# Optimization experiments

Measured on AMD Instinct MI355X. Metric: run time of the kernel, lower is better.

## Reference

```python
import jax, jax.numpy as jnp
import numpy as np

B, N, C, K = 2, 4096, 128, 16
EPS = 1e-5


def _conv(w, b, x):
    # 1x1 Conv2d == per-point channel mix: w [O,I], x [B,I,N,K]
    return jnp.einsum('oi,bink->bonk', w, x) + b[None, :, None, None]


def _bn(x, g, be):
    # training-mode BatchNorm2d: biased stats over (B, N, K) per channel
    m = jnp.mean(x, axis=(0, 2, 3), keepdims=True)
    v = jnp.var(x, axis=(0, 2, 3), keepdims=True)
    return g[None, :, None, None] * (x - m) * jax.lax.rsqrt(v + EPS) + be[None, :, None, None]


def setup_inputs() -> dict:
    key = jax.random.key(0)
    ks = jax.random.split(key, 24)

    def w(k_, o, i):
        return jax.random.normal(k_, (o, i), jnp.float32) * (1.0 / np.sqrt(i))

    def b(k_, o):
        return jax.random.normal(k_, (o,), jnp.float32) * 0.01

    return {
        'xyz': jax.random.normal(ks[0], (B, 3, N), jnp.float32),
        'features': jax.random.normal(ks[1], (B, C, N), jnp.float32),
        'w_theta1': w(ks[2], C, 3), 'b_theta1': b(ks[3], C),
        'w_theta2': w(ks[4], C, C), 'b_theta2': b(ks[5], C),
        'g_theta': jnp.ones((C,), jnp.float32), 'beta_theta': jnp.zeros((C,), jnp.float32),
        'w_phi': w(ks[6], C, C), 'b_phi': b(ks[7], C),
        'w_psi': w(ks[8], C, C), 'b_psi': b(ks[9], C),
        'w_alpha': w(ks[10], C, C), 'b_alpha': b(ks[11], C),
        'w_gamma1': w(ks[12], C, C), 'b_gamma1': b(ks[13], C),
        'w_gamma2': w(ks[14], C, C), 'b_gamma2': b(ks[15], C),
        'g_gamma': jnp.ones((C,), jnp.float32), 'beta_gamma': jnp.zeros((C,), jnp.float32),
        'k': K,
    }


def reference(xyz, features, w_theta1, b_theta1, w_theta2, b_theta2, g_theta, beta_theta,
              w_phi, b_phi, w_psi, b_psi, w_alpha, b_alpha,
              w_gamma1, b_gamma1, w_gamma2, b_gamma2, g_gamma, beta_gamma, k):
    Bv, _, Nv = xyz.shape
    # --- knn on coordinates: negative squared distances, top-k neighbors ---
    xx = jnp.sum(xyz * xyz, axis=1, keepdims=True)                 # [B,1,N]
    inner = -2.0 * jnp.einsum('bcn,bcm->bnm', xyz, xyz)            # [B,N,N]
    dist = -xx - inner - jnp.swapaxes(xx, 1, 2)                    # -||xi-xj||^2
    idx = jax.lax.top_k(dist, k)[1]                                # [B,N,K]

    bidx = jnp.arange(Bv)[:, None, None]
    xt = jnp.swapaxes(xyz, 1, 2)                                   # [B,N,3]
    nbr_x = xt[bidx, idx]                                          # [B,N,K,3]
    pos = jnp.transpose(xt[:, :, None, :] - nbr_x, (0, 3, 1, 2))   # [B,3,N,K]
    ft = jnp.swapaxes(features, 1, 2)                              # [B,N,C]
    x_j = jnp.transpose(ft[bidx, idx], (0, 3, 1, 2))               # [B,C,N,K]

    # delta = relu(BN(theta2(theta1(pos))))
    delta = jax.nn.relu(_bn(_conv(w_theta2, b_theta2, _conv(w_theta1, b_theta1, pos)), g_theta, beta_theta))
    # phi(x_i): conv is per-point, so compute on [B,C,N] and broadcast over K
    lin_xi = (jnp.einsum('oi,bin->bon', w_phi, features) + b_phi[None, :, None])[..., None]
    lin_xj = _conv(w_psi, b_psi, x_j)
    rel = lin_xi - lin_xj + delta
    rel = jax.nn.relu(_bn(_conv(w_gamma2, b_gamma2, _conv(w_gamma1, b_gamma1, rel)), g_gamma, beta_gamma))
    weights = jax.nn.softmax(rel, axis=-1)                         # softmax over K
    feats = _conv(w_alpha, b_alpha, x_j) + delta
    return jnp.sum(weights * feats, axis=-1)                       # [B,C,N]
```

## Files before the change

kernel.cpp:

```cpp
#include <hip/hip_runtime.h>
#include <math.h>

typedef __attribute__((ext_vector_type(8))) short short8;
typedef __attribute__((ext_vector_type(4))) float f32x4;
typedef unsigned short u16;
typedef unsigned long long u64;

#define NNPTS 131072
#define NQ    8192

__device__ __forceinline__ u16 f2bf(float f) {
  unsigned u = __float_as_uint(f);
  u = u + 0x7fffu + ((u >> 16) & 1u);
  return (u16)(u >> 16);
}
__device__ __forceinline__ float bf2f(u16 h) {
  return __uint_as_float(((unsigned)h) << 16);
}
__device__ __forceinline__ unsigned fkey(float f) {
  unsigned u = __float_as_uint(f);
  return u ^ (((unsigned)((int)u >> 31)) | 0x80000000u);
}

__device__ __forceinline__ unsigned wave_max_u32(unsigned v) {
  unsigned t;
  t = (unsigned)__builtin_amdgcn_update_dpp(0, (int)v, 0x111, 0xf, 0xf, true); v = v > t ? v : t;
  t = (unsigned)__builtin_amdgcn_update_dpp(0, (int)v, 0x112, 0xf, 0xf, true); v = v > t ? v : t;
  t = (unsigned)__builtin_amdgcn_update_dpp(0, (int)v, 0x114, 0xf, 0xf, true); v = v > t ? v : t;
  t = (unsigned)__builtin_amdgcn_update_dpp(0, (int)v, 0x118, 0xf, 0xf, true); v = v > t ? v : t;
  t = (unsigned)__builtin_amdgcn_update_dpp(0, (int)v, 0x142, 0xf, 0xf, true); v = v > t ? v : t;
  t = (unsigned)__builtin_amdgcn_update_dpp(0, (int)v, 0x143, 0xf, 0xf, true); v = v > t ? v : t;
  return (unsigned)__builtin_amdgcn_readlane((int)v, 63);
}

__global__ __launch_bounds__(256) void front_kernel(
    const float* __restrict__ xyz, const float* __restrict__ f,
    const float* __restrict__ wphi, const float* __restrict__ wpsi,
    const float* __restrict__ walpha,
    const float* __restrict__ wg1, const float* __restrict__ wg2,
    const float* __restrict__ bg1, const float* __restrict__ bg2,
    const float* __restrict__ wt1, const float* __restrict__ bt1,
    const float* __restrict__ wt2, const float* __restrict__ bt2,
    u16* __restrict__ featB,
    u16* __restrict__ WphiB, u16* __restrict__ WpsiB, u16* __restrict__ WalphaB,
    u16* __restrict__ WfusB, float* __restrict__ c0v,
    float* __restrict__ Wc, float* __restrict__ bc,
    int* __restrict__ idxOut)
{
  __shared__ float sh[4160];
  int bid = blockIdx.x, tid = threadIdx.x;

  if (bid < 2048) {
    float* xxS = sh;
    int lane = tid & 63, wid = tid >> 6;
    int q = bid*4 + wid;
    int b = q >> 12, n = q & 4095;
    const float* X = xyz + (size_t)b * 12288;
    for (int t = tid; t < 4096; t += 256) {
      float mx = X[t], my = X[4096+t], mz = X[8192+t];
      xxS[t] = __fadd_rn(__fadd_rn(__fmul_rn(mx,mx), __fmul_rn(my,my)), __fmul_rn(mz,mz));
    }
    __syncthreads();
    float qx = X[n], qy = X[4096+n], qz = X[8192+n];
    float xxq = xxS[n];

    float v0=-INFINITY, v1=-INFINITY, v2=-INFINITY, v3=-INFINITY;
    int   i0=0x7fffffff, i1=0x7fffffff, i2=0x7fffffff, i3=0x7fffffff;
    u64 alive = ~0ull;

    #pragma unroll 8
    for (int j = 0; j < 64; ++j) {
      int m = j*64 + lane;
      float mx = X[m], my = X[4096+m], mz = X[8192+m];
      float xxm = xxS[m];
      float dot = __fadd_rn(__fadd_rn(__fmul_rn(qx,mx), __fmul_rn(qy,my)), __fmul_rn(qz,mz));
      float inner = __fmul_rn(-2.0f, dot);
      float dv = __fsub_rn(__fsub_rn(-xxm, inner), xxq);
      bool c0_=dv>v0, c1_=dv>v1, c2_=dv>v2, c3_=dv>v3;
      int ni1 = c0_ ? i0 : (c1_ ? m : i1);
      int ni2 = c1_ ? i1 : (c2_ ? m : i2);
      int ni3 = c2_ ? i2 : (c3_ ? m : i3);
      i0 = c0_ ? m : i0;
      i1 = ni1; i2 = ni2; i3 = ni3;
      float nv1 = __builtin_amdgcn_fmed3f(dv, v0, v1);
      float nv2 = __builtin_amdgcn_fmed3f(dv, v1, v2);
      float nv3 = __builtin_amdgcn_fmed3f(dv, v2, v3);
      v0 = fmaxf(v0, dv);
      v1 = nv1; v2 = nv2; v3 = nv3;
    }

    int cnt = 4;
    for (int r = 0; r < 16; ++r) {
      unsigned hi = fkey(v0);
      unsigned ghi = wave_max_u32(hi);
      u64 bal = __ballot(hi == ghi);
      unsigned gi;
      if (__builtin_popcountll(bal) == 1) {
        int ln = (int)__builtin_ctzll(bal);
        gi = (unsigned)__builtin_amdgcn_readlane(i0, ln);
      } else {
        unsigned lo = (hi == ghi) ? (0xFFFFFFFFu - (unsigned)i0) : 0u;
        gi = 0xFFFFFFFFu - wave_max_u32(lo);
      }
      if (lane == 0) idxOut[(size_t)q*16 + r] = (int)gi;
      if ((int)(gi & 63) == lane) {
        alive &= ~(1ull << (gi >> 6));
        v0=v1; i0=i1; v1=v2; i1=i2; v2=v3; i2=i3; v3=-INFINITY; i3=0x7fffffff;
        if (--cnt == 0 && r < 15) {
          v0=v1=v2=v3=-INFINITY; i0=i1=i2=i3=0x7fffffff;
          for (int j2 = 0; j2 < 64; ++j2) {
            if (!((alive >> j2) & 1ull)) continue;
            int m = j2*64 + lane;
            float mx = X[m], my = X[4096+m], mz = X[8192+m];
            float xxm = xxS[m];
            float dot = __fadd_rn(__fadd_rn(__fmul_rn(qx,mx), __fmul_rn(qy,my)), __fmul_rn(qz,mz));
            float inner = __fmul_rn(-2.0f, dot);
            float dv = __fsub_rn(__fsub_rn(-xxm, inner), xxq);
            bool c0_=dv>v0, c1_=dv>v1, c2_=dv>v2, c3_=dv>v3;
            int ni1 = c0_ ? i0 : (c1_ ? m : i1);
            int ni2 = c1_ ? i1 : (c2_ ? m : i2);
            int ni3 = c2_ ? i2 : (c3_ ? m : i3);
            i0 = c0_ ? m : i0;
            i1 = ni1; i2 = ni2; i3 = ni3;
            float nv1 = __builtin_amdgcn_fmed3f(dv, v0, v1);
            float nv2 = __builtin_amdgcn_fmed3f(dv, v1, v2);
            float nv3 = __builtin_amdgcn_fmed3f(dv, v2, v3);
            v0 = fmaxf(v0, dv);
            v1 = nv1; v2 = nv2; v3 = nv3;
          }
          cnt = 4;
        }
      }
    }
  } else if (bid < 2304) {
    float (*T)[65] = (float(*)[65])sh;
    int t = bid - 2048;
    int tx = tid & 63, tg = tid >> 6;
    int n0 = (t & 63) * 64, c0_ = ((t >> 6) & 1) * 64, b = t >> 7;
    const float* src = f + ((size_t)b * 128 + c0_) * 4096 + n0;
    #pragma unroll
    for (int it = 0; it < 16; ++it) {
      int cl = tg + it * 4;
      T[cl][tx] = src[(size_t)cl * 4096 + tx];
    }
    __syncthreads();
    u16* dst = featB + ((size_t)b * 4096 + n0) * 128 + c0_;
    #pragma unroll
    for (int it = 0; it < 16; ++it) {
      int nl = tg + it * 4;
      dst[(size_t)nl * 128 + tx] = f2bf(T[tx][nl]);
    }
  } else {
    int cc = bid - 2304;
    if (tid < 128) {
      int i = tid;
      WphiB[cc*128+i]   = f2bf(wphi[cc*128+i]);
      WpsiB[cc*128+i]   = f2bf(wpsi[cc*128+i]);
      WalphaB[cc*128+i] = f2bf(walpha[cc*128+i]);
      float s = 0.f;
      for (int t = 0; t < 128; ++t) s = fmaf(wg2[cc*128+t], wg1[t*128+i], s);
      WfusB[cc*128+i] = f2bf(s);
      if (i == 0) {
        float s0 = bg2[cc];
        for (int t = 0; t < 128; ++t) s0 = fmaf(wg2[cc*128+t], bg1[t], s0);
        c0v[cc] = s0;
        for (int j = 0; j < 3; ++j) {
          float a = 0.f;
          for (int t = 0; t < 128; ++t) a = fmaf(wt2[cc*128+t], wt1[t*3+j], a);
          Wc[cc*3+j] = a;
        }
        float bb = bt2[cc];
        for (int t = 0; t < 128; ++t) bb = fmaf(wt2[cc*128+t], bt1[t], bb);
        bc[cc] = bb;
      }
    }
  }
}

__device__ __forceinline__ void theta_fold_c(const double* __restrict__ stS,
                                             const float* __restrict__ Wc,
                                             const float* __restrict__ bc,
                                             const float* __restrict__ gth,
                                             const float* __restrict__ bth,
                                             int c, float* w0o, float* w1o,
                                             float* w2o, float* bdo)
{
  const double cnt = (double)NNPTS;
  double m0 = stS[0]/cnt, m1 = stS[1]/cnt, m2 = stS[2]/cnt;
  double Pxx = stS[3]/cnt, Pxy = stS[4]/cnt, Pxz = stS[5]/cnt;
  double Pyy = stS[6]/cnt, Pyz = stS[7]/cnt, Pzz = stS[8]/cnt;
  double w0 = Wc[c*3], w1 = Wc[c*3+1], w2 = Wc[c*3+2], bb = bc[c];
  double wm = w0*m0 + w1*m1 + w2*m2;
  double mu = wm + bb;
  double quad = w0*(Pxx*w0 + Pxy*w1 + Pxz*w2)
              + w1*(Pxy*w0 + Pyy*w1 + Pyz*w2)
              + w2*(Pxz*w0 + Pyz*w1 + Pzz*w2);
  double Ex2 = quad + 2.0*bb*wm + bb*bb;
  double var = Ex2 - mu*mu;
  double s = (double)gth[c] / sqrt(var + 1e-5);
  double t = (double)bth[c] - s*mu;
  *w0o = (float)(s*w0);
  *w1o = (float)(s*w1);
  *w2o = (float)(s*w2);
  *bdo = (float)(s*bb + t);
}

__device__ __forceinline__ void zero_acc(f32x4 a[2][4]) {
  #pragma unroll
  for (int mt = 0; mt < 2; ++mt)
    #pragma unroll
    for (int nt = 0; nt < 4; ++nt)
      a[mt][nt] = (f32x4){0.f, 0.f, 0.f, 0.f};
}

__device__ __forceinline__ void load_af(const u16* __restrict__ WB, int m0, int row, int g,
                                        short8 a[2][4]) {
  #pragma unroll
  for (int mt = 0; mt < 2; ++mt)
    #pragma unroll
    for (int kc = 0; kc < 4; ++kc)
      a[mt][kc] = *(const short8*)&WB[(size_t)(m0 + mt*16 + row)*128 + kc*32 + g*8];
}

__device__ __forceinline__ void gemm64(const short8 a[2][4], const uint4* __restrict__ Xs4,
                                       int row, int g, f32x4 acc[2][4]) {
  #pragma unroll
  for (int kc = 0; kc < 4; ++kc) {
    #pragma unroll
    for (int nt = 0; nt < 4; ++nt) {
      int p = nt*16 + row;
      short8 bfr = *(const short8*)&Xs4[p*16 + ((kc*4 + g) ^ (p & 7))];
      acc[0][nt] = __builtin_amdgcn_mfma_f32_16x16x32_bf16(a[0][kc], bfr, acc[0][nt], 0, 0, 0);
      acc[1][nt] = __builtin_amdgcn_mfma_f32_16x16x32_bf16(a[1][kc], bfr, acc[1][nt], 0, 0, 0);
    }
  }
}

__global__ __launch_bounds__(256) void mid_kernel(
    const u16* __restrict__ featB,
    const u16* __restrict__ WphiB, const u16* __restrict__ WpsiB,
    const u16* __restrict__ WalphaB,
    const float* __restrict__ bphi, const float* __restrict__ bpsi,
    const float* __restrict__ balpha,
    float* __restrict__ linxi, float* __restrict__ psiP, float* __restrict__ alphaP,
    const float* __restrict__ xyz, const int* __restrict__ idx,
    double* __restrict__ part)
{
  __shared__ uint4 Xs4[64*16];
  __shared__ double rd[256];
  int bid = blockIdx.x, tid = threadIdx.x;

  if (bid < 128) {
    int lane = tid & 63, wid = tid >> 6;
    int row = lane & 15, g = lane >> 4, m0 = wid * 32;
    size_t g0 = (size_t)bid * 64;
    for (int u = tid; u < 1024; u += 256) {
      int p = u >> 4, seg = u & 15;
      Xs4[p*16 + (seg ^ (p & 7))] = *(const uint4*)&featB[(g0 + p)*128 + seg*8];
    }
    __syncthreads();
    const u16* Ws[3]    = {WphiB, WpsiB, WalphaB};
    const float* bs[3]  = {bphi, bpsi, balpha};
    float* outs[3]      = {linxi, psiP, alphaP};
    #pragma unroll
    for (int w = 0; w < 3; ++w) {
      short8 afr[2][4];
      load_af(Ws[w], m0, row, g, afr);
      f32x4 acc[2][4];
      zero_acc(acc);
      gemm64(afr, Xs4, row, g, acc);
      #pragma unroll
      for (int mt = 0; mt < 2; ++mt) {
        int c = m0 + mt*16 + g*4;
        float4 bp = *(const float4*)&bs[w][c];
        const float* bpp = (const float*)&bp;
        #pragma unroll
        for (int nt = 0; nt < 4; ++nt) {
          int p = nt*16 + row;
          float4 v = make_float4(acc[mt][nt][0]+bpp[0], acc[mt][nt][1]+bpp[1],
                                 acc[mt][nt][2]+bpp[2], acc[mt][nt][3]+bpp[3]);
          *(float4*)&outs[w][(g0 + p)*128 + c] = v;
        }
      }
    }
  } else {
    int bid2 = bid - 128;
    int qg = bid2*256 + tid;
    int b = qg >> 12, n = qg & 4095;
    const float* X = xyz + (size_t)b * 12288;
    float qx = X[n], qy = X[4096+n], qz = X[8192+n];
    double l[9] = {0,0,0,0,0,0,0,0,0};
    for (int kk = 0; kk < 16; ++kk) {
      int nb = idx[(size_t)qg*16 + kk];
      float px = qx - X[nb], py = qy - X[4096+nb], pz = qz - X[8192+nb];
      l[0] += px; l[1] += py; l[2] += pz;
      l[3] += (double)px*px; l[4] += (double)px*py; l[5] += (double)px*pz;
      l[6] += (double)py*py; l[7] += (double)py*pz; l[8] += (double)pz*pz;
    }
    for (int j = 0; j < 9; ++j) {
      __syncthreads();
      rd[tid] = l[j];
      __syncthreads();
      for (int s = 128; s > 0; s >>= 1) {
        if (tid < s) rd[tid] += rd[tid + s];
        __syncthreads();
      }
      if (tid == 0) part[(size_t)bid2*9 + j] = rd[0];
    }
  }
}

__global__ __launch_bounds__(256) void gamma_part(const float* __restrict__ gs,
                                                  const float* __restrict__ gq,
                                                  double* __restrict__ partS,
                                                  double* __restrict__ partQ)
{
  int c = threadIdx.x & 127;
  int arr = threadIdx.x >> 7;
  int j = blockIdx.x;
  const float* src = arr ? gq : gs;
  double s = 0.0;
  #pragma unroll 8
  for (int bk = j*32; bk < j*32 + 32; ++bk)
    s += src[(size_t)bk*128 + c];
  (arr ? partQ : partS)[(size_t)j*128 + c] = s;
}

__global__ __launch_bounds__(256) void fused_pass(
    const float* __restrict__ psiP, const float* __restrict__ linxi,
    const int* __restrict__ idx, const float* __restrict__ xyz,
    const u16* __restrict__ WfusB, const float* __restrict__ c0,
    const double* __restrict__ part, const float* __restrict__ Wc,
    const float* __restrict__ bc, const float* __restrict__ gth,
    const float* __restrict__ bth,
    u16* __restrict__ g2W,
    float* __restrict__ gs, float* __restrict__ gq)
{
  __shared__ uint4 XsR[64*16];
  __shared__ float LxS[4][128];
  __shared__ float WdS[4][128];
  __shared__ float posS[3][64];
  __shared__ int   pidx[64];
  __shared__ float redS[128], redQ[128];
  __shared__ double stS[9];

  int tid = threadIdx.x, lane = tid & 63, wid = tid >> 6;
  int row = lane & 15, g = lane >> 4;
  int m0 = wid * 32;
  int q0 = blockIdx.x * 4, b = q0 >> 12;
  int n0 = q0 & 4095;
  const float* X = xyz + (size_t)b * 12288;
  size_t b12 = (size_t)b << 12;

  if (tid < 64) {
    int q = tid >> 4;
    int nb = idx[(size_t)(q0 + q)*16 + (tid & 15)];
    pidx[tid] = nb;
    int nq = n0 + q;
    posS[0][tid] = X[nq]      - X[nb];
    posS[1][tid] = X[4096+nq] - X[4096+nb];
    posS[2][tid] = X[8192+nq] - X[8192+nb];
  } else if (tid < 73) {
    int j = tid - 64;
    double s = 0.0;
    for (int bk = 0; bk < 32; ++bk) s += part[(size_t)bk*9 + j];
    stS[j] = s;
  }
  for (int u = tid; u < 512; u += 256)
    LxS[u >> 7][u & 127] = linxi[(size_t)q0*128 + u];
  __syncthreads();
  if (tid < 128) {
    float a0, a1, a2, a3;
    theta_fold_c(stS, Wc, bc, gth, bth, tid, &a0, &a1, &a2, &a3);
    WdS[0][tid] = a0; WdS[1][tid] = a1; WdS[2][tid] = a2; WdS[3][tid] = a3;
  }
  __syncthreads();

  #pragma unroll
  for (int it = 0; it < 4; ++it) {
    int u = tid + it*256;
    int p = u >> 4, seg = u & 15;
    int q = p >> 4, cc = seg * 8;
    float p0 = posS[0][p], p1 = posS[1][p], p2 = posS[2][p];
    const float* psir = &psiP[(b12 + (size_t)pidx[p])*128 + cc];
    float ps[8];
    *(float4*)&ps[0] = *(const float4*)&psir[0];
    *(float4*)&ps[4] = *(const float4*)&psir[4];
    ushort4 lohi[2];
    u16* wv = (u16*)lohi;
    #pragma unroll
    for (int r = 0; r < 8; ++r) {
      int c = cc + r;
      float d = fmaf(WdS[2][c], p2, fmaf(WdS[1][c], p1, fmaf(WdS[0][c], p0, WdS[3][c])));
      d = fmaxf(d, 0.f);
      wv[r] = f2bf(LxS[q][c] - ps[r] + d);
    }
    XsR[p*16 + (seg ^ (p & 7))] = *(uint4*)lohi;
  }
  __syncthreads();

  short8 afr[2][4];
  f32x4 acc[2][4];
  load_af(WfusB, m0, row, g, afr);
  zero_acc(acc);
  gemm64(afr, XsR, row, g, acc);

  #pragma unroll
  for (int mt = 0; mt < 2; ++mt) {
    int c = m0 + mt*16 + g*4;
    float4 c0v = *(const float4*)&c0[c];
    const float* c0p = (const float*)&c0v;
    float sv[4], qv[4];
    #pragma unroll
    for (int r = 0; r < 4; ++r) { sv[r] = 0.f; qv[r] = 0.f; }
    #pragma unroll
    for (int nt = 0; nt < 4; ++nt) {
      size_t gbase = ((size_t)(q0 + nt)*128 + c)*16 + row;
      #pragma unroll
      for (int r = 0; r < 4; ++r) {
        float gg = acc[mt][nt][r] + c0p[r];
        g2W[gbase + (size_t)r*16] = f2bf(gg);
        sv[r] += gg; qv[r] = fmaf(gg, gg, qv[r]);
      }
    }
    #pragma unroll
    for (int r = 0; r < 4; ++r) {
      #pragma unroll
      for (int d = 1; d < 16; d <<= 1) {
        sv[r] += __shfl_xor(sv[r], d);
        qv[r] += __shfl_xor(qv[r], d);
      }
    }
    if (row == 0) {
      *(float4*)&redS[c] = make_float4(sv[0], sv[1], sv[2], sv[3]);
      *(float4*)&redQ[c] = make_float4(qv[0], qv[1], qv[2], qv[3]);
    }
  }
  __syncthreads();
  if (tid < 128) {
    gs[(size_t)blockIdx.x*128 + tid] = redS[tid];
    gq[(size_t)blockIdx.x*128 + tid] = redQ[tid];
  }
}

__global__ __launch_bounds__(256) void out_kernel(const u16* __restrict__ g2W,
                                                  const float* __restrict__ alphaP,
                                                  const int* __restrict__ idx,
                                                  const float* __restrict__ xyz,
                                                  const double* __restrict__ part,
                                                  const float* __restrict__ Wc,
                                                  const float* __restrict__ bc,
                                                  const float* __restrict__ gth,
                                                  const float* __restrict__ bth,
                                                  const double* __restrict__ partS,
                                                  const double* __restrict__ partQ,
                                                  const float* __restrict__ gga,
                                                  const float* __restrict__ bga,
                                                  float* __restrict__ out)
{
  __shared__ int   pidxO[16][16];
  __shared__ float posO[3][16][16];
  __shared__ float prmS[6][64];
  __shared__ float resS[64][18];
  __shared__ double stS[9];
  int tid = threadIdx.x;
  int cblk = blockIdx.x & 1;
  int qblk = blockIdx.x >> 1;
  int c0 = cblk * 64;
  int lc = tid & 63;
  int c = c0 + lc;
  int qg = tid >> 6;
  int q0 = qblk * 16;
  int bb = q0 >> 12;
  int n0 = q0 & 4095;
  size_t bOff = (size_t)bb << 12;
  const float* X = xyz + (size_t)bb * 12288;
  {
    int q = tid >> 4, k = tid & 15;
    int gq = q0 + q;
    int nq = gq & 4095;
    int nb = idx[(size_t)gq*16 + k];
    pidxO[q][k] = nb;
    posO[0][q][k] = X[nq]      - X[nb];
    posO[1][q][k] = X[4096+nq] - X[4096+nb];
    posO[2][q][k] = X[8192+nq] - X[8192+nb];
  }
  if (tid < 9) {
    int j = tid;
    double s = 0.0;
    for (int bk = 0; bk < 32; ++bk) s += part[(size_t)bk*9 + j];
    stS[j] = s;
  }
  __syncthreads();
  if (tid < 64) {
    int cc = c0 + tid;
    double S = 0.0, Q = 0.0;
    #pragma unroll 8
    for (int j = 0; j < 64; ++j) {
      S += partS[(size_t)j*128 + cc];
      Q += partQ[(size_t)j*128 + cc];
    }
    const double cntd = (double)NNPTS;
    double md = S/cntd, vd = Q/cntd - md*md;
    double sd = (double)gga[cc] / sqrt(vd + 1e-5);
    prmS[0][tid] = (float)sd;
    prmS[1][tid] = (float)((double)bga[cc] - sd*md);
    float a0, a1, a2, a3;
    theta_fold_c(stS, Wc, bc, gth, bth, cc, &a0, &a1, &a2, &a3);
    prmS[2][tid] = a0; prmS[3][tid] = a1; prmS[4][tid] = a2; prmS[5][tid] = a3;
  }
  __syncthreads();
  float s  = prmS[0][lc], t   = prmS[1][lc];
  float w0 = prmS[2][lc], w1  = prmS[3][lc];
  float w2 = prmS[4][lc], bdv = prmS[5][lc];
  #pragma unroll
  for (int qi = 0; qi < 4; ++qi) {
    int ql = qi*4 + qg;
    int gq = q0 + ql;
    size_t base2 = ((size_t)gq*128 + c)*16;
    uint4 ga = *(const uint4*)&g2W[base2];
    uint4 gb = *(const uint4*)&g2W[base2 + 8];
    unsigned gw[8] = {ga.x, ga.y, ga.z, ga.w, gb.x, gb.y, gb.z, gb.w};
    float se = 0.f, so = 0.f;
    #pragma unroll
    for (int k = 0; k < 16; ++k) {
      u16 hv = (u16)((gw[k >> 1] >> ((k & 1) * 16)) & 0xFFFFu);
      float rel = fmaxf(fmaf(s, bf2f(hv), t), 0.f);
      float e = expf(rel);
      float d = fmaf(w2, posO[2][ql][k], fmaf(w1, posO[1][ql][k], fmaf(w0, posO[0][ql][k], bdv)));
      d = fmaxf(d, 0.f);
      float F = alphaP[(bOff + (size_t)pidxO[ql][k])*128 + c] + d;
      se += e; so = fmaf(e, F, so);
    }
    resS[lc][ql] = so / se;
  }
  __syncthreads();
  if (tid < 128) {
    int lc2 = tid >> 1, half = tid & 1;
    int c2 = c0 + lc2;
    float* dst = &out[(((size_t)bb*128 + c2) << 12) + n0 + half*8];
    float4 v0 = make_float4(resS[lc2][half*8+0], resS[lc2][half*8+1],
                            resS[lc2][half*8+2], resS[lc2][half*8+3]);
    float4 v1 = make_float4(resS[lc2][half*8+4], resS[lc2][half*8+5],
                            resS[lc2][half*8+6], resS[lc2][half*8+7]);
    *(float4*)&dst[0] = v0;
    *(float4*)&dst[4] = v1;
  }
}

extern "C" void kernel_launch(void* const* d_in, const int* in_sizes, int n_in,
                              void* d_out, int out_size, void* d_ws, size_t ws_size,
                              hipStream_t stream)
{
  const float* xyz      = (const float*)d_in[0];
  const float* features = (const float*)d_in[1];
  const float* wt1      = (const float*)d_in[2];
  const float* bt1      = (const float*)d_in[3];
  const float* wt2      = (const float*)d_in[4];
  const float* bt2      = (const float*)d_in[5];
  const float* gth      = (const float*)d_in[6];
  const float* bth      = (const float*)d_in[7];
  const float* wphi     = (const float*)d_in[8];
  const float* bphi     = (const float*)d_in[9];
  const float* wpsi     = (const float*)d_in[10];
  const float* bpsi     = (const float*)d_in[11];
  const float* walpha   = (const float*)d_in[12];
  const float* balpha   = (const float*)d_in[13];
  const float* wg1      = (const float*)d_in[14];
  const float* bg1      = (const float*)d_in[15];
  const float* wg2      = (const float*)d_in[16];
  const float* bg2      = (const float*)d_in[17];
  const float* gga      = (const float*)d_in[18];
  const float* bga      = (const float*)d_in[19];

  char* w = (char*)d_ws;
  size_t off = 0;
  auto take = [&](size_t bytes) -> void* {
    void* p = w + off;
    off = (off + bytes + 255) & ~(size_t)255;
    return p;
  };
  int*    idxW    = (int*)   take((size_t)NQ*16*4);
  u16*    featB   = (u16*)   take((size_t)NQ*128*2);
  float*  linxi   = (float*) take((size_t)NQ*128*4);
  float*  psiP    = (float*) take((size_t)NQ*128*4);
  float*  alphaP  = (float*) take((size_t)NQ*128*4);
  u16*    WphiB   = (u16*)   take(32768);
  u16*    WpsiB   = (u16*)   take(32768);
  u16*    WalphaB = (u16*)   take(32768);
  u16*    WfusB   = (u16*)   take(32768);
  float*  c0      = (float*) take(512);
  float*  Wc      = (float*) take(1536);
  float*  bc      = (float*) take(512);
  double* part    = (double*)take(32*9*8);
  float*  gs      = (float*) take((size_t)2048*128*4);
  float*  gq      = (float*) take((size_t)2048*128*4);
  double* partS   = (double*)take((size_t)64*128*8);
  double* partQ   = (double*)take((size_t)64*128*8);
  u16*    g2W     = (u16*)   take((size_t)NNPTS*128*2);
  float*  out     = (float*)d_out;

  front_kernel<<<2432, 256, 0, stream>>>(xyz, features,
      wphi, wpsi, walpha, wg1, wg2, bg1, bg2, wt1, bt1, wt2, bt2,
      featB, WphiB, WpsiB, WalphaB, WfusB, c0, Wc, bc, idxW);
  mid_kernel<<<160, 256, 0, stream>>>(featB, WphiB, WpsiB, WalphaB,
      bphi, bpsi, balpha, linxi, psiP, alphaP, xyz, idxW, part);
  fused_pass<<<2048, 256, 0, stream>>>(psiP, linxi, idxW, xyz,
      WfusB, c0, part, Wc, bc, gth, bth, g2W, gs, gq);
  gamma_part<<<64, 256, 0, stream>>>(gs, gq, partS, partQ);
  out_kernel<<<1024, 256, 0, stream>>>(g2W, alphaP, idxW, xyz,
      part, Wc, bc, gth, bth, partS, partQ, gga, bga, out);
}
```

Before: 119.0 us.

## Fuse per-point phi/psi/alpha GEMMs into front kernel, drop bf16 staging buffers

Moves the per-point feature GEMMs (phi, psi, alpha) out of mid_kernel and into the front kernel's transpose blocks. Those blocks now build the swizzled bf16 feature tile in shared memory and convert the weights on the fly, so the featB and bf16 weight buffers are no longer written or read back. The GEMMs run alongside the knn blocks instead of in a later launch, and the leftover pos-stat reduction becomes a small separate kernel. In exchange, each GEMM block now transposes all 128 channels, the front kernel needs twice the shared memory, and every block re-converts the weights.

```diff
diff --git a/kernel.cpp b/kernel.cpp
--- a/kernel.cpp
+++ b/kernel.cpp
@@ -33,21 +33,71 @@
   return (unsigned)__builtin_amdgcn_readlane((int)v, 63);
 }
 
+__device__ __forceinline__ void zero_acc(f32x4 a[2][4]) {
+  #pragma unroll
+  for (int mt = 0; mt < 2; ++mt)
+    #pragma unroll
+    for (int nt = 0; nt < 4; ++nt)
+      a[mt][nt] = (f32x4){0.f, 0.f, 0.f, 0.f};
+}
+
+__device__ __forceinline__ void load_af(const u16* __restrict__ WB, int m0, int row, int g,
+                                        short8 a[2][4]) {
+  #pragma unroll
+  for (int mt = 0; mt < 2; ++mt)
+    #pragma unroll
+    for (int kc = 0; kc < 4; ++kc)
+      a[mt][kc] = *(const short8*)&WB[(size_t)(m0 + mt*16 + row)*128 + kc*32 + g*8];
+}
+
+__device__ __forceinline__ void load_af_f32(const float* __restrict__ W, int m0, int row, int g,
+                                            short8 a[2][4]) {
+  #pragma unroll
+  for (int mt = 0; mt < 2; ++mt)
+    #pragma unroll
+    for (int kc = 0; kc < 4; ++kc) {
+      int base = (m0 + mt*16 + row)*128 + kc*32 + g*8;
+      float4 f0 = *(const float4*)&W[base];
+      float4 f1 = *(const float4*)&W[base + 4];
+      short8 v;
+      v[0] = (short)f2bf(f0.x); v[1] = (short)f2bf(f0.y);
+      v[2] = (short)f2bf(f0.z); v[3] = (short)f2bf(f0.w);
+      v[4] = (short)f2bf(f1.x); v[5] = (short)f2bf(f1.y);
+      v[6] = (short)f2bf(f1.z); v[7] = (short)f2bf(f1.w);
+      a[mt][kc] = v;
+    }
+}
+
+__device__ __forceinline__ void gemm64(const short8 a[2][4], const uint4* __restrict__ Xs4,
+                                       int row, int g, f32x4 acc[2][4]) {
+  #pragma unroll
+  for (int kc = 0; kc < 4; ++kc) {
+    #pragma unroll
+    for (int nt = 0; nt < 4; ++nt) {
+      int p = nt*16 + row;
+      short8 bfr = *(const short8*)&Xs4[p*16 + ((kc*4 + g) ^ (p & 7))];
+      acc[0][nt] = __builtin_amdgcn_mfma_f32_16x16x32_bf16(a[0][kc], bfr, acc[0][nt], 0, 0, 0);
+      acc[1][nt] = __builtin_amdgcn_mfma_f32_16x16x32_bf16(a[1][kc], bfr, acc[1][nt], 0, 0, 0);
+    }
+  }
+}
+
 __global__ __launch_bounds__(256) void front_kernel(
     const float* __restrict__ xyz, const float* __restrict__ f,
     const float* __restrict__ wphi, const float* __restrict__ wpsi,
     const float* __restrict__ walpha,
+    const float* __restrict__ bphi, const float* __restrict__ bpsi,
+    const float* __restrict__ balpha,
     const float* __restrict__ wg1, const float* __restrict__ wg2,
     const float* __restrict__ bg1, const float* __restrict__ bg2,
     const float* __restrict__ wt1, const float* __restrict__ bt1,
     const float* __restrict__ wt2, const float* __restrict__ bt2,
-    u16* __restrict__ featB,
-    u16* __restrict__ WphiB, u16* __restrict__ WpsiB, u16* __restrict__ WalphaB,
     u16* __restrict__ WfusB, float* __restrict__ c0v,
     float* __restrict__ Wc, float* __restrict__ bc,
+    float* __restrict__ linxi, float* __restrict__ psiP, float* __restrict__ alphaP,
     int* __restrict__ idxOut)
 {
-  __shared__ float sh[4160];
+  __shared__ float sh[8320];
   int bid = blockIdx.x, tid = threadIdx.x;
 
   if (bid < 2048) {
@@ -132,31 +182,64 @@
         }
       }
     }
-  } else if (bid < 2304) {
-    float (*T)[65] = (float(*)[65])sh;
-    int t = bid - 2048;
+  } else if (bid < 2176) {
+    float (*T)[66] = (float(*)[66])sh;
+    u16* XsB = (u16*)&sh[4224];
+    int pg = bid - 2048;
+    int b = pg >> 6;
+    int n0 = (pg & 63) * 64;
+    size_t g0 = (size_t)pg * 64;
     int tx = tid & 63, tg = tid >> 6;
-    int n0 = (t & 63) * 64, c0_ = ((t >> 6) & 1) * 64, b = t >> 7;
-    const float* src = f + ((size_t)b * 128 + c0_) * 4096 + n0;
-    #pragma unroll
-    for (int it = 0; it < 16; ++it) {
-      int cl = tg + it * 4;
-      T[cl][tx] = src[(size_t)cl * 4096 + tx];
-    }
-    __syncthreads();
-    u16* dst = featB + ((size_t)b * 4096 + n0) * 128 + c0_;
-    #pragma unroll
-    for (int it = 0; it < 16; ++it) {
-      int nl = tg + it * 4;
-      dst[(size_t)nl * 128 + tx] = f2bf(T[tx][nl]);
+    const float* src = f + ((size_t)b * 128) * 4096 + n0;
+    #pragma unroll
+    for (int half = 0; half < 2; ++half) {
+      #pragma unroll
+      for (int it = 0; it < 16; ++it) {
+        int cl = tg + it * 4;
+        T[cl][tx] = src[(size_t)(half*64 + cl) * 4096 + tx];
+      }
+      __syncthreads();
+      for (int u = tid; u < 512; u += 256) {
+        int p = u >> 3, s8 = u & 7;
+        int seg = half*8 + s8;
+        ushort4 w2v[2];
+        u16* wv = (u16*)w2v;
+        #pragma unroll
+        for (int r = 0; r < 8; ++r) wv[r] = f2bf(T[s8*8 + r][p]);
+        *(uint4*)&XsB[((size_t)p*16 + (seg ^ (p & 7))) * 8] = *(uint4*)w2v;
+      }
+      __syncthreads();
+    }
+    int lane = tid & 63, wid = tid >> 6;
+    int row = lane & 15, g = lane >> 4, m0 = wid * 32;
+    const float* Ws[3]   = {wphi, wpsi, walpha};
+    const float* bs[3]   = {bphi, bpsi, balpha};
+    float* outs[3]       = {linxi, psiP, alphaP};
+    #pragma unroll
+    for (int w = 0; w < 3; ++w) {
+      short8 afr[2][4];
+      load_af_f32(Ws[w], m0, row, g, afr);
+      f32x4 acc[2][4];
+      zero_acc(acc);
+      gemm64(afr, (const uint4*)XsB, row, g, acc);
+      #pragma unroll
+      for (int mt = 0; mt < 2; ++mt) {
+        int c = m0 + mt*16 + g*4;
+        float4 bp = *(const float4*)&bs[w][c];
+        const float* bpp = (const float*)&bp;
+        #pragma unroll
+        for (int nt = 0; nt < 4; ++nt) {
+          int p = nt*16 + row;
+          float4 v = make_float4(acc[mt][nt][0]+bpp[0], acc[mt][nt][1]+bpp[1],
+                                 acc[mt][nt][2]+bpp[2], acc[mt][nt][3]+bpp[3]);
+          *(float4*)&outs[w][(g0 + p)*128 + c] = v;
+        }
+      }
     }
   } else {
-    int cc = bid - 2304;
+    int cc = bid - 2176;
     if (tid < 128) {
       int i = tid;
-      WphiB[cc*128+i]   = f2bf(wphi[cc*128+i]);
-      WpsiB[cc*128+i]   = f2bf(wpsi[cc*128+i]);
-      WalphaB[cc*128+i] = f2bf(walpha[cc*128+i]);
       float s = 0.f;
       for (int t = 0; t < 128; ++t) s = fmaf(wg2[cc*128+t], wg1[t*128+i], s);
       WfusB[cc*128+i] = f2bf(s);
@@ -205,108 +288,32 @@
   *bdo = (float)(s*bb + t);
 }
 
-__device__ __forceinline__ void zero_acc(f32x4 a[2][4]) {
-  #pragma unroll
-  for (int mt = 0; mt < 2; ++mt)
-    #pragma unroll
-    for (int nt = 0; nt < 4; ++nt)
-      a[mt][nt] = (f32x4){0.f, 0.f, 0.f, 0.f};
-}
-
-__device__ __forceinline__ void load_af(const u16* __restrict__ WB, int m0, int row, int g,
-                                        short8 a[2][4]) {
-  #pragma unroll
-  for (int mt = 0; mt < 2; ++mt)
-    #pragma unroll
-    for (int kc = 0; kc < 4; ++kc)
-      a[mt][kc] = *(const short8*)&WB[(size_t)(m0 + mt*16 + row)*128 + kc*32 + g*8];
-}
-
-__device__ __forceinline__ void gemm64(const short8 a[2][4], const uint4* __restrict__ Xs4,
-                                       int row, int g, f32x4 acc[2][4]) {
-  #pragma unroll
-  for (int kc = 0; kc < 4; ++kc) {
-    #pragma unroll
-    for (int nt = 0; nt < 4; ++nt) {
-      int p = nt*16 + row;
-      short8 bfr = *(const short8*)&Xs4[p*16 + ((kc*4 + g) ^ (p & 7))];
-      acc[0][nt] = __builtin_amdgcn_mfma_f32_16x16x32_bf16(a[0][kc], bfr, acc[0][nt], 0, 0, 0);
-      acc[1][nt] = __builtin_amdgcn_mfma_f32_16x16x32_bf16(a[1][kc], bfr, acc[1][nt], 0, 0, 0);
-    }
-  }
-}
-
-__global__ __launch_bounds__(256) void mid_kernel(
-    const u16* __restrict__ featB,
-    const u16* __restrict__ WphiB, const u16* __restrict__ WpsiB,
-    const u16* __restrict__ WalphaB,
-    const float* __restrict__ bphi, const float* __restrict__ bpsi,
-    const float* __restrict__ balpha,
-    float* __restrict__ linxi, float* __restrict__ psiP, float* __restrict__ alphaP,
-    const float* __restrict__ xyz, const int* __restrict__ idx,
-    double* __restrict__ part)
+__global__ __launch_bounds__(256) void pos_kernel(const float* __restrict__ xyz,
+                                                  const int* __restrict__ idx,
+                                                  double* __restrict__ part)
 {
-  __shared__ uint4 Xs4[64*16];
   __shared__ double rd[256];
-  int bid = blockIdx.x, tid = threadIdx.x;
-
-  if (bid < 128) {
-    int lane = tid & 63, wid = tid >> 6;
-    int row = lane & 15, g = lane >> 4, m0 = wid * 32;
-    size_t g0 = (size_t)bid * 64;
-    for (int u = tid; u < 1024; u += 256) {
-      int p = u >> 4, seg = u & 15;
-      Xs4[p*16 + (seg ^ (p & 7))] = *(const uint4*)&featB[(g0 + p)*128 + seg*8];
-    }
+  int qg = blockIdx.x*256 + threadIdx.x;
+  int b = qg >> 12, n = qg & 4095;
+  const float* X = xyz + (size_t)b * 12288;
+  float qx = X[n], qy = X[4096+n], qz = X[8192+n];
+  double l[9] = {0,0,0,0,0,0,0,0,0};
+  for (int kk = 0; kk < 16; ++kk) {
+    int nb = idx[(size_t)qg*16 + kk];
+    float px = qx - X[nb], py = qy - X[4096+nb], pz = qz - X[8192+nb];
+    l[0] += px; l[1] += py; l[2] += pz;
+    l[3] += (double)px*px; l[4] += (double)px*py; l[5] += (double)px*pz;
+    l[6] += (double)py*py; l[7] += (double)py*pz; l[8] += (double)pz*pz;
+  }
+  for (int j = 0; j < 9; ++j) {
     __syncthreads();
-    const u16* Ws[3]    = {WphiB, WpsiB, WalphaB};
-    const float* bs[3]  = {bphi, bpsi, balpha};
-    float* outs[3]      = {linxi, psiP, alphaP};
-    #pragma unroll
-    for (int w = 0; w < 3; ++w) {
-      short8 afr[2][4];
-      load_af(Ws[w], m0, row, g, afr);
-      f32x4 acc[2][4];
-      zero_acc(acc);
-      gemm64(afr, Xs4, row, g, acc);
-      #pragma unroll
-      for (int mt = 0; mt < 2; ++mt) {
-        int c = m0 + mt*16 + g*4;
-        float4 bp = *(const float4*)&bs[w][c];
-        const float* bpp = (const float*)&bp;
-        #pragma unroll
-        for (int nt = 0; nt < 4; ++nt) {
-          int p = nt*16 + row;
-          float4 v = make_float4(acc[mt][nt][0]+bpp[0], acc[mt][nt][1]+bpp[1],
-                                 acc[mt][nt][2]+bpp[2], acc[mt][nt][3]+bpp[3]);
-          *(float4*)&outs[w][(g0 + p)*128 + c] = v;
-        }
-      }
-    }
-  } else {
-    int bid2 = bid - 128;
-    int qg = bid2*256 + tid;
-    int b = qg >> 12, n = qg & 4095;
-    const float* X = xyz + (size_t)b * 12288;
-    float qx = X[n], qy = X[4096+n], qz = X[8192+n];
-    double l[9] = {0,0,0,0,0,0,0,0,0};
-    for (int kk = 0; kk < 16; ++kk) {
-      int nb = idx[(size_t)qg*16 + kk];
-      float px = qx - X[nb], py = qy - X[4096+nb], pz = qz - X[8192+nb];
-      l[0] += px; l[1] += py; l[2] += pz;
-      l[3] += (double)px*px; l[4] += (double)px*py; l[5] += (double)px*pz;
-      l[6] += (double)py*py; l[7] += (double)py*pz; l[8] += (double)pz*pz;
-    }
-    for (int j = 0; j < 9; ++j) {
+    rd[threadIdx.x] = l[j];
+    __syncthreads();
+    for (int s = 128; s > 0; s >>= 1) {
+      if (threadIdx.x < s) rd[threadIdx.x] += rd[threadIdx.x + s];
       __syncthreads();
-      rd[tid] = l[j];
-      __syncthreads();
-      for (int s = 128; s > 0; s >>= 1) {
-        if (tid < s) rd[tid] += rd[tid + s];
-        __syncthreads();
-      }
-      if (tid == 0) part[(size_t)bid2*9 + j] = rd[0];
-    }
+    }
+    if (threadIdx.x == 0) part[(size_t)blockIdx.x*9 + j] = rd[0];
   }
 }
 
@@ -581,13 +588,9 @@
     return p;
   };
   int*    idxW    = (int*)   take((size_t)NQ*16*4);
-  u16*    featB   = (u16*)   take((size_t)NQ*128*2);
   float*  linxi   = (float*) take((size_t)NQ*128*4);
   float*  psiP    = (float*) take((size_t)NQ*128*4);
   float*  alphaP  = (float*) take((size_t)NQ*128*4);
-  u16*    WphiB   = (u16*)   take(32768);
-  u16*    WpsiB   = (u16*)   take(32768);
-  u16*    WalphaB = (u16*)   take(32768);
   u16*    WfusB   = (u16*)   take(32768);
   float*  c0      = (float*) take(512);
   float*  Wc      = (float*) take(1536);
@@ -600,11 +603,11 @@
   u16*    g2W     = (u16*)   take((size_t)NNPTS*128*2);
   float*  out     = (float*)d_out;
 
-  front_kernel<<<2432, 256, 0, stream>>>(xyz, features,
-      wphi, wpsi, walpha, wg1, wg2, bg1, bg2, wt1, bt1, wt2, bt2,
-      featB, WphiB, WpsiB, WalphaB, WfusB, c0, Wc, bc, idxW);
-  mid_kernel<<<160, 256, 0, stream>>>(featB, WphiB, WpsiB, WalphaB,
-      bphi, bpsi, balpha, linxi, psiP, alphaP, xyz, idxW, part);
+  front_kernel<<<2304, 256, 0, stream>>>(xyz, features,
+      wphi, wpsi, walpha, bphi, bpsi, balpha,
+      wg1, wg2, bg1, bg2, wt1, bt1, wt2, bt2,
+      WfusB, c0, Wc, bc, linxi, psiP, alphaP, idxW);
+  pos_kernel<<<32, 256, 0, stream>>>(xyz, idxW, part);
   fused_pass<<<2048, 256, 0, stream>>>(psiP, linxi, idxW, xyz,
       WfusB, c0, part, Wc, bc, gth, bth, g2W, gs, gq);
   gamma_part<<<64, 256, 0, stream>>>(gs, gq, partS, partQ);
```

New measurement: 122.4 us. +2.9%, slower.
